# Performance work log

Measured on AMD Instinct MI355X. Metric: run time of the kernel, lower is better.

## Reference

```python
import jax, jax.numpy as jnp
import numpy as np

EPS = 1e-15
MAX_ATANH = 1.0 - 1e-5
V = 2097152   # total nodes (B*N*L flattened)
E = 8388608   # edges, ~avg degree 4 (temporal + parent/child)
ATT = 16
MAXD = 512    # mixer embedding table size
# curvature c = 1.0 (registered buffer, constant)


def _mobius_add(a, b):
    # Poincare ball Mobius addition, c = 1
    a2 = jnp.sum(a * a, -1, keepdims=True)
    b2 = jnp.sum(b * b, -1, keepdims=True)
    ab = jnp.sum(a * b, -1, keepdims=True)
    num = (1.0 + 2.0 * ab + b2) * a + (1.0 - a2) * b
    den = 1.0 + 2.0 * ab + a2 * b2
    return num / jnp.maximum(den, EPS)


def _log_map_x(x, y):
    # log_x(y): tangent vector at x pointing to y (c = 1)
    sub = _mobius_add(-x, y)
    n = jnp.maximum(jnp.linalg.norm(sub, axis=-1, keepdims=True), EPS)
    lam = 2.0 / jnp.maximum(1.0 - jnp.sum(x * x, -1, keepdims=True), EPS)
    return (2.0 / lam) * jnp.arctanh(jnp.minimum(n, MAX_ATANH)) * (sub / n)


def _exp_map_x(x, v):
    # exp_x(v) (c = 1)
    n = jnp.maximum(jnp.linalg.norm(v, axis=-1, keepdims=True), EPS)
    lam = 2.0 / jnp.maximum(1.0 - jnp.sum(x * x, -1, keepdims=True), EPS)
    return _mobius_add(x, jnp.tanh(0.5 * lam * n) * (v / n))


def setup_inputs() -> dict:
    key = jax.random.key(0)
    ks = jax.random.split(key, 8)
    # node embeddings strictly inside the unit ball: exp0 of a small tangent vec
    v0 = 0.5 * jax.random.normal(ks[0], (V, 2), jnp.float32)
    n0 = jnp.maximum(jnp.linalg.norm(v0, axis=-1, keepdims=True), EPS)
    x = jnp.tanh(n0) * v0 / n0
    edge_index = jax.random.randint(ks[1], (2, E), 0, V)
    depth = jax.random.randint(ks[2], (V,), 0, MAXD)
    W1 = jax.random.normal(ks[3], (2, ATT), jnp.float32) / jnp.sqrt(2.0)
    b1 = 0.1 * jax.random.normal(ks[4], (ATT,), jnp.float32)
    W2 = jax.random.normal(ks[5], (ATT, 1), jnp.float32) / jnp.sqrt(float(ATT))
    eta = jnp.float32(1.0)
    depth_scale = 1.0 + 0.01 * jax.random.normal(ks[6], (MAXD,), jnp.float32)
    depth_theta = 0.01 * jax.random.normal(ks[7], (MAXD,), jnp.float32)
    return {"x": x, "W1": W1, "b1": b1, "W2": W2, "eta": eta,
            "depth_scale": depth_scale, "depth_theta": depth_theta,
            "edge_index": edge_index, "depth": depth}


def reference(x, W1, b1, W2, eta, depth_scale, depth_theta, edge_index, depth):
    row, col = edge_index[0], edge_index[1]
    xi = x[row]                      # [E,2] gather target endpoints
    xj = x[col]                      # [E,2] gather source endpoints
    v_ij = _log_map_x(xi, xj)        # [E,2] hyperbolic log-map
    # small per-edge MLP scorer: Linear(2,16) -> GELU(exact) -> Linear(16,1)
    h = jax.nn.gelu(v_ij @ W1 + b1, approximate=False)
    scores = (h @ W2)[:, 0]          # [E]
    # segment softmax over target node (row)
    mx = jax.ops.segment_max(scores, row, num_segments=V)
    e = jnp.exp(scores - mx[row])
    den = jax.ops.segment_sum(e, row, num_segments=V)
    alpha = e / jnp.maximum(den[row], EPS)
    # scatter-add aggregate in tangent space
    m = jax.ops.segment_sum(alpha[:, None] * v_ij, row, num_segments=V)  # [V,2]
    # depth-gated mixer: per-node scale + 2D rotation
    d = jnp.minimum(depth, MAXD - 1)
    k = depth_scale[d][:, None]
    ang = depth_theta[d]
    ca, sa = jnp.cos(ang), jnp.sin(ang)
    m = k * jnp.stack([ca * m[:, 0] - sa * m[:, 1],
                       sa * m[:, 0] + ca * m[:, 1]], axis=-1)
    # exp-map update
    return _exp_map_x(x, eta * m)
```

## Files before the change

### kernel.cpp

```cpp
#include <hip/hip_runtime.h>
#include <math.h>

#define EPSF 1e-15f
#define MAX_ATANH (1.0f - 1e-5f)
#define ATT 16

#define LOG_NPB 11
#define NPB (1 << LOG_NPB)
#define MAXB 1024
#define NBLK 512
#define NPR 1024

#define TDIM 512
#define TSPAN 12.5f
#define TSTEP (TSPAN / (float)(TDIM - 1))
#define TSCALE ((float)(TDIM - 1) / TSPAN)
#define TOFF (6.25f * TSCALE)

__device__ __forceinline__ float fast_atanh(float z) {
    return 0.5f * __logf(__fdividef(1.0f + z, 1.0f - z));
}
__device__ __forceinline__ float fast_tanh(float z) {
    return 1.0f - __fdividef(2.0f, __expf(2.0f * z) + 1.0f);
}
__device__ __forceinline__ float gelu_exact(float u) {
    return 0.5f * u * (1.0f + erff(u * 0.70710678118654752f));
}

__global__ void __launch_bounds__(256) build_table_kernel(
        const float* __restrict__ W1, const float* __restrict__ b1,
        const float* __restrict__ W2, float2* __restrict__ tab) {
    const int idx = blockIdx.x * 256 + threadIdx.x;
    if (idx >= TDIM * TDIM) return;
    const int iy = idx >> 9;
    const int ix = idx & (TDIM - 1);
    const float vy  = fmaf((float)iy, TSTEP, -6.25f);
    const float vx0 = fmaf((float)ix, TSTEP, -6.25f);
    const float vx1 = fmaf((float)min(ix + 1, TDIM - 1), TSTEP, -6.25f);
    float s0 = 0.0f, s1 = 0.0f;
    #pragma unroll
    for (int k = 0; k < ATT; ++k) {
        const float w1x = W1[k], w1y = W1[ATT + k], bb = b1[k], w2 = W2[k];
        s0 = fmaf(gelu_exact(fmaf(vx0, w1x, fmaf(vy, w1y, bb))), w2, s0);
        s1 = fmaf(gelu_exact(fmaf(vx1, w1x, fmaf(vy, w1y, bb))), w2, s1);
    }
    tab[idx] = make_float2(s0, s1);
}

__global__ void __launch_bounds__(256) hist_kernel(const int* __restrict__ row,
                                                   int E, int B,
                                                   unsigned* __restrict__ counts ) {
    __shared__ unsigned h[MAXB];
    for (int i = threadIdx.x; i < B; i += 256) h[i] = 0u;
    __syncthreads();
    const int T = gridDim.x * 256;
    const int nv = E >> 2;
    const int4* row4 = (const int4*)row;
    for (int i = blockIdx.x * 256 + threadIdx.x; i < nv; i += T) {
        const int4 r = row4[i];
        atomicAdd(&h[((unsigned)r.x) >> LOG_NPB], 1u);
        atomicAdd(&h[((unsigned)r.y) >> LOG_NPB], 1u);
        atomicAdd(&h[((unsigned)r.z) >> LOG_NPB], 1u);
        atomicAdd(&h[((unsigned)r.w) >> LOG_NPB], 1u);
    }
    for (int e = (nv << 2) + blockIdx.x * 256 + threadIdx.x; e < E; e += T)
        atomicAdd(&h[((unsigned)row[e]) >> LOG_NPB], 1u);
    __syncthreads();
    for (int i = threadIdx.x; i < B; i += 256)
        counts[(size_t)i * gridDim.x + blockIdx.x] = h[i];
}

__global__ void __launch_bounds__(256) scan_blocks_kernel(const unsigned* __restrict__ counts,
                                                          unsigned* __restrict__ within,
                                                          unsigned* __restrict__ totals) {
    const int b = blockIdx.x;
    const unsigned* src = counts + (size_t)b * NBLK;
    unsigned* dst = within + (size_t)b * NBLK;
    __shared__ unsigned s[256];
    unsigned v0, v1;
    {
        const uint2 v = ((const uint2*)src)[threadIdx.x];
        v0 = v.x; v1 = v.y;
    }
    s[threadIdx.x] = v0 + v1;
    __syncthreads();
    for (int off = 1; off < 256; off <<= 1) {
        unsigned t = (threadIdx.x >= off) ? s[threadIdx.x - off] : 0u;
        __syncthreads();
        s[threadIdx.x] += t;
        __syncthreads();
    }
    unsigned base = (threadIdx.x > 0) ? s[threadIdx.x - 1] : 0u;
    uint2 o;
    o.x = base; o.y = base + v0;
    ((uint2*)dst)[threadIdx.x] = o;
    if (threadIdx.x == 255) totals[b] = s[255];
}

__global__ void __launch_bounds__(256) scan_totals_kernel(const unsigned* __restrict__ totals,
                                                          unsigned* __restrict__ base, int B) {
    __shared__ unsigned s[256];
    unsigned vals[8];
    const int i0 = threadIdx.x * 8;
    unsigned sum = 0u;
    #pragma unroll
    for (int k = 0; k < 8; ++k) {
        vals[k] = (i0 + k < B) ? totals[i0 + k] : 0u;
        sum += vals[k];
    }
    s[threadIdx.x] = sum;
    __syncthreads();
    for (int off = 1; off < 256; off <<= 1) {
        unsigned t = (threadIdx.x >= off) ? s[threadIdx.x - off] : 0u;
        __syncthreads();
        s[threadIdx.x] += t;
        __syncthreads();
    }
    unsigned b0 = (threadIdx.x > 0) ? s[threadIdx.x - 1] : 0u;
    #pragma unroll
    for (int k = 0; k < 8; ++k) {
        if (i0 + k < B) base[i0 + k] = b0;
        b0 += vals[k];
    }
    if (threadIdx.x == 255) base[B] = s[255];
}

__global__ void __launch_bounds__(256) scatter_kernel(const int* __restrict__ row,
                                                      const int* __restrict__ col,
                                                      int E, int B,
                                                      const unsigned* __restrict__ base,
                                                      const unsigned* __restrict__ within,
                                                      unsigned* __restrict__ payload) {
    __shared__ unsigned cur[MAXB];
    const int nblk = gridDim.x;
    for (int i = threadIdx.x; i < B; i += 256)
        cur[i] = base[i] + within[(size_t)i * nblk + blockIdx.x];
    __syncthreads();
    const int T = nblk * 256;
    const int nv = E >> 2;
    const int4* row4 = (const int4*)row;
    const int4* col4 = (const int4*)col;
    for (int i = blockIdx.x * 256 + threadIdx.x; i < nv; i += T) {
        const int4 r = row4[i];
        const int4 c = col4[i];
        {
            const unsigned rr = (unsigned)r.x;
            const unsigned pos = atomicAdd(&cur[rr >> LOG_NPB], 1u);
            payload[pos] = ((rr & (NPB - 1)) << 21) | (unsigned)c.x;
        }
        {
            const unsigned rr = (unsigned)r.y;
            const unsigned pos = atomicAdd(&cur[rr >> LOG_NPB], 1u);
            payload[pos] = ((rr & (NPB - 1)) << 21) | (unsigned)c.y;
        }
        {
            const unsigned rr = (unsigned)r.z;
            const unsigned pos = atomicAdd(&cur[rr >> LOG_NPB], 1u);
            payload[pos] = ((rr & (NPB - 1)) << 21) | (unsigned)c.z;
        }
        {
            const unsigned rr = (unsigned)r.w;
            const unsigned pos = atomicAdd(&cur[rr >> LOG_NPB], 1u);
            payload[pos] = ((rr & (NPB - 1)) << 21) | (unsigned)c.w;
        }
    }
    for (int e = (nv << 2) + blockIdx.x * 256 + threadIdx.x; e < E; e += T) {
        const unsigned rr = (unsigned)row[e];
        const unsigned pos = atomicAdd(&cur[rr >> LOG_NPB], 1u);
        payload[pos] = ((rr & (NPB - 1)) << 21) | (unsigned)col[e];
    }
}

__device__ __forceinline__ void edge_single(unsigned p,
        const float2* __restrict__ x, const float2* __restrict__ tab,
        const float2* sxi, float* sden, float* smx, float* smy) {
    const unsigned lrow = (p >> 21) & (NPR - 1);
    const unsigned c = p & 0x1FFFFFu;
    const float2 xj = x[c];
    const float2 xi = sxi[lrow];

    const float ax = -xi.x, ay = -xi.y;
    const float bx = xj.x,  by = xj.y;
    const float a2 = ax * ax + ay * ay;
    const float b2 = bx * bx + by * by;
    const float ab = ax * bx + ay * by;
    const float ca = 1.0f + 2.0f * ab + b2;
    const float cb = 1.0f - a2;
    const float dn = fmaxf(1.0f + 2.0f * ab + a2 * b2, EPSF);
    const float rdn = __fdividef(1.0f, dn);
    const float subx = (ca * ax + cb * bx) * rdn;
    const float suby = (ca * ay + cb * by) * rdn;

    const float n = fmaxf(sqrtf(subx * subx + suby * suby), EPSF);
    const float M = fmaxf(1.0f - (xi.x * xi.x + xi.y * xi.y), EPSF);
    const float scl = M * fast_atanh(fminf(n, MAX_ATANH)) * __fdividef(1.0f, n);
    const float vx = scl * subx;
    const float vy = scl * suby;

    float tx = fmaf(vx, TSCALE, TOFF);
    float ty = fmaf(vy, TSCALE, TOFF);
    tx = fminf(fmaxf(tx, 0.0f), 510.999f);
    ty = fminf(fmaxf(ty, 0.0f), 510.999f);
    const int ix = (int)tx;
    const int iy = (int)ty;
    const float fx = tx - (float)ix;
    const float fy = ty - (float)iy;
    const int baseIdx = (iy << 9) + ix;
    const float2 r0 = tab[baseIdx];
    const float2 r1 = tab[baseIdx + TDIM];
    const float s0 = fmaf(fx, r0.y - r0.x, r0.x);
    const float s1 = fmaf(fx, r1.y - r1.x, r1.x);
    const float s  = fmaf(fy, s1 - s0, s0);

    const float ee = __expf(s);
    atomicAdd(&sden[lrow], ee);
    atomicAdd(&smx[lrow], ee * vx);
    atomicAdd(&smy[lrow], ee * vy);
}

__global__ void __launch_bounds__(512, 8) bucket_reduce_kernel(
        const float2* __restrict__ x,
        const float2* __restrict__ tab,
        const unsigned* __restrict__ base,
        const unsigned* __restrict__ payload,
        const int* __restrict__ depth,
        const float* __restrict__ depth_scale,
        const float* __restrict__ depth_theta,
        const float* __restrict__ eta_p,
        float2* __restrict__ out, int V) {
    __shared__ float  sden[NPR];
    __shared__ float  smx[NPR];
    __shared__ float  smy[NPR];
    __shared__ float2 sxi[NPR];
    const int bkt = blockIdx.x >> 1;
    const unsigned hb = blockIdx.x & 1;
    const int nodeBase = (bkt << LOG_NPB) + ((int)hb << 10);
    for (int i = threadIdx.x; i < NPR; i += 512) {
        sden[i] = 0.f; smx[i] = 0.f; smy[i] = 0.f;
        sxi[i] = x[nodeBase + i];
    }
    __syncthreads();

    const unsigned e0 = base[bkt], e1 = base[bkt + 1];
    for (unsigned e = e0 + threadIdx.x; e < e1; e += 512) {
        const unsigned p = payload[e];
        if ((p >> 31) == hb)
            edge_single(p, x, tab, sxi, sden, smx, smy);
    }
    __syncthreads();

    const float eta = eta_p[0];
    for (int i = threadIdx.x; i < NPR; i += 512) {
        const int v = nodeBase + i;
        if (v >= V) break;
        const float rdv = __fdividef(1.0f, fmaxf(sden[i], EPSF));
        const float mx = smx[i] * rdv;
        const float my = smy[i] * rdv;

        const int d = min(depth[v], 511);
        const float k   = depth_scale[d];
        const float ang = depth_theta[d];
        const float cs = __cosf(ang), sn = __sinf(ang);
        const float m0 = eta * (k * (cs * mx - sn * my));
        const float m1 = eta * (k * (sn * mx + cs * my));

        const float2 xi = sxi[i];

        const float n = fmaxf(sqrtf(m0 * m0 + m1 * m1), EPSF);
        const float M = fmaxf(1.0f - (xi.x * xi.x + xi.y * xi.y), EPSF);
        const float t = fast_tanh(__fdividef(n, M));
        const float tn = t * __fdividef(1.0f, n);
        const float bx = tn * m0;
        const float by = tn * m1;

        const float a2 = xi.x * xi.x + xi.y * xi.y;
        const float b2 = bx * bx + by * by;
        const float ab = xi.x * bx + xi.y * by;
        const float ca = 1.0f + 2.0f * ab + b2;
        const float cb = 1.0f - a2;
        const float dn = fmaxf(1.0f + 2.0f * ab + a2 * b2, EPSF);
        const float rdn = __fdividef(1.0f, dn);

        out[v] = make_float2((ca * xi.x + cb * bx) * rdn,
                             (ca * xi.y + cb * by) * rdn);
    }
}

extern "C" void kernel_launch(void* const* d_in, const int* in_sizes, int n_in,
                              void* d_out, int out_size, void* d_ws, size_t ws_size,
                              hipStream_t stream) {
    const float2* x          = (const float2*)d_in[0];
    const float*  W1         = (const float*)d_in[1];
    const float*  b1         = (const float*)d_in[2];
    const float*  W2         = (const float*)d_in[3];
    const float*  eta        = (const float*)d_in[4];
    const float*  dscale     = (const float*)d_in[5];
    const float*  dtheta     = (const float*)d_in[6];
    const int*    edge_index = (const int*)d_in[7];
    const int*    depth      = (const int*)d_in[8];

    const int V = in_sizes[0] / 2;
    const int E = in_sizes[7] / 2;
    const int B = (V + NPB - 1) >> LOG_NPB;

    const int* row = edge_index;
    const int* col = edge_index + E;

    unsigned* payload = (unsigned*)d_ws;
    unsigned* counts  = payload + E;
    unsigned* within  = counts + (size_t)B * NBLK;
    unsigned* totals  = within + (size_t)B * NBLK;
    unsigned* base    = totals + B;
    float2*   tab     = (float2*)within;

    hist_kernel<<<NBLK, 256, 0, stream>>>(row, E, B, counts);
    scan_blocks_kernel<<<B, 256, 0, stream>>>(counts, within, totals);
    scan_totals_kernel<<<1, 256, 0, stream>>>(totals, base, B);
    scatter_kernel<<<NBLK, 256, 0, stream>>>(row, col, E, B, base, within, payload);
    build_table_kernel<<<(TDIM * TDIM) / 256, 256, 0, stream>>>(W1, b1, W2, tab);
    bucket_reduce_kernel<<<2 * B, 512, 0, stream>>>(x, tab, base, payload,
                                                    depth, dscale, dtheta, eta,
                                                    (float2*)d_out, V);
}
```

Measured before the change: 261.6 us.

## Split 2048-node buckets into 1024-node halves before reduction

Adds a split pass that partitions each 2048-node bucket's edge payload into two 1024-node sub-buckets using a finer histogram and scan. Each reduce block then reads only its own edges instead of scanning the whole bucket and discarding half. The aim is to remove the duplicated payload read and the divergent filter, at the cost of an extra kernel pass that reads and writes the full payload with contended shared atomics.

```diff
diff --git a/kernel.cpp b/kernel.cpp
--- a/kernel.cpp
+++ b/kernel.cpp
@@ -5,11 +5,13 @@
 #define MAX_ATANH (1.0f - 1e-5f)
 #define ATT 16
 
-#define LOG_NPB 11
-#define NPB (1 << LOG_NPB)
-#define MAXB 1024
+#define LOG_NPR 10
+#define NPR (1 << LOG_NPR)
+#define LOG_NPM 11
+#define NPM (1 << LOG_NPM)
+#define B2MAX 2048
+#define BMMAX 1024
 #define NBLK 512
-#define NPR 1024
 
 #define TDIM 512
 #define TSPAN 12.5f
@@ -48,41 +50,41 @@
 }
 
 __global__ void __launch_bounds__(256) hist_kernel(const int* __restrict__ row,
-                                                   int E, int B,
-                                                   unsigned* __restrict__ counts ) {
-    __shared__ unsigned h[MAXB];
-    for (int i = threadIdx.x; i < B; i += 256) h[i] = 0u;
+                                                   int E, int B2,
+                                                   unsigned* __restrict__ counts2 ) {
+    __shared__ unsigned h[B2MAX];
+    for (int i = threadIdx.x; i < B2; i += 256) h[i] = 0u;
     __syncthreads();
     const int T = gridDim.x * 256;
     const int nv = E >> 2;
     const int4* row4 = (const int4*)row;
     for (int i = blockIdx.x * 256 + threadIdx.x; i < nv; i += T) {
         const int4 r = row4[i];
-        atomicAdd(&h[((unsigned)r.x) >> LOG_NPB], 1u);
-        atomicAdd(&h[((unsigned)r.y) >> LOG_NPB], 1u);
-        atomicAdd(&h[((unsigned)r.z) >> LOG_NPB], 1u);
-        atomicAdd(&h[((unsigned)r.w) >> LOG_NPB], 1u);
+        atomicAdd(&h[((unsigned)r.x) >> LOG_NPR], 1u);
+        atomicAdd(&h[((unsigned)r.y) >> LOG_NPR], 1u);
+        atomicAdd(&h[((unsigned)r.z) >> LOG_NPR], 1u);
+        atomicAdd(&h[((unsigned)r.w) >> LOG_NPR], 1u);
     }
     for (int e = (nv << 2) + blockIdx.x * 256 + threadIdx.x; e < E; e += T)
-        atomicAdd(&h[((unsigned)row[e]) >> LOG_NPB], 1u);
-    __syncthreads();
-    for (int i = threadIdx.x; i < B; i += 256)
-        counts[(size_t)i * gridDim.x + blockIdx.x] = h[i];
-}
-
-__global__ void __launch_bounds__(256) scan_blocks_kernel(const unsigned* __restrict__ counts,
+        atomicAdd(&h[((unsigned)row[e]) >> LOG_NPR], 1u);
+    __syncthreads();
+    for (int i = threadIdx.x; i < B2; i += 256)
+        counts2[(size_t)i * gridDim.x + blockIdx.x] = h[i];
+}
+
+__global__ void __launch_bounds__(256) scan_blocks_kernel(const unsigned* __restrict__ counts2,
                                                           unsigned* __restrict__ within,
-                                                          unsigned* __restrict__ totals) {
+                                                          unsigned* __restrict__ totals2) {
     const int b = blockIdx.x;
-    const unsigned* src = counts + (size_t)b * NBLK;
-    unsigned* dst = within + (size_t)b * NBLK;
+    const uint2 r0 = ((const uint2*)(counts2 + (size_t)(2 * b)     * NBLK))[threadIdx.x];
+    const uint2 r1 = ((const uint2*)(counts2 + (size_t)(2 * b + 1) * NBLK))[threadIdx.x];
+    const unsigned c0 = r0.x + r1.x;
+    const unsigned c1 = r0.y + r1.y;
     __shared__ unsigned s[256];
-    unsigned v0, v1;
-    {
-        const uint2 v = ((const uint2*)src)[threadIdx.x];
-        v0 = v.x; v1 = v.y;
-    }
-    s[threadIdx.x] = v0 + v1;
+    __shared__ unsigned sa[256], sb[256];
+    s[threadIdx.x] = c0 + c1;
+    sa[threadIdx.x] = r0.x + r0.y;
+    sb[threadIdx.x] = r1.x + r1.y;
     __syncthreads();
     for (int off = 1; off < 256; off <<= 1) {
         unsigned t = (threadIdx.x >= off) ? s[threadIdx.x - off] : 0u;
@@ -92,20 +94,25 @@
     }
     unsigned base = (threadIdx.x > 0) ? s[threadIdx.x - 1] : 0u;
     uint2 o;
-    o.x = base; o.y = base + v0;
-    ((uint2*)dst)[threadIdx.x] = o;
-    if (threadIdx.x == 255) totals[b] = s[255];
-}
-
-__global__ void __launch_bounds__(256) scan_totals_kernel(const unsigned* __restrict__ totals,
-                                                          unsigned* __restrict__ base, int B) {
+    o.x = base; o.y = base + c0;
+    ((uint2*)(within + (size_t)b * NBLK))[threadIdx.x] = o;
+    for (int off = 128; off > 0; off >>= 1) {
+        if (threadIdx.x < off) { sa[threadIdx.x] += sa[threadIdx.x + off];
+                                 sb[threadIdx.x] += sb[threadIdx.x + off]; }
+        __syncthreads();
+    }
+    if (threadIdx.x == 0) { totals2[2 * b] = sa[0]; totals2[2 * b + 1] = sb[0]; }
+}
+
+__global__ void __launch_bounds__(256) scan_totals_kernel(const unsigned* __restrict__ totals2,
+                                                          unsigned* __restrict__ base2, int B2) {
     __shared__ unsigned s[256];
     unsigned vals[8];
     const int i0 = threadIdx.x * 8;
     unsigned sum = 0u;
     #pragma unroll
     for (int k = 0; k < 8; ++k) {
-        vals[k] = (i0 + k < B) ? totals[i0 + k] : 0u;
+        vals[k] = (i0 + k < B2) ? totals2[i0 + k] : 0u;
         sum += vals[k];
     }
     s[threadIdx.x] = sum;
@@ -119,22 +126,22 @@
     unsigned b0 = (threadIdx.x > 0) ? s[threadIdx.x - 1] : 0u;
     #pragma unroll
     for (int k = 0; k < 8; ++k) {
-        if (i0 + k < B) base[i0 + k] = b0;
+        if (i0 + k < B2) base2[i0 + k] = b0;
         b0 += vals[k];
     }
-    if (threadIdx.x == 255) base[B] = s[255];
+    if (threadIdx.x == 255) base2[B2] = s[255];
 }
 
 __global__ void __launch_bounds__(256) scatter_kernel(const int* __restrict__ row,
                                                       const int* __restrict__ col,
-                                                      int E, int B,
-                                                      const unsigned* __restrict__ base,
+                                                      int E, int BM,
+                                                      const unsigned* __restrict__ base2,
                                                       const unsigned* __restrict__ within,
                                                       unsigned* __restrict__ payload) {
-    __shared__ unsigned cur[MAXB];
+    __shared__ unsigned cur[BMMAX];
     const int nblk = gridDim.x;
-    for (int i = threadIdx.x; i < B; i += 256)
-        cur[i] = base[i] + within[(size_t)i * nblk + blockIdx.x];
+    for (int i = threadIdx.x; i < BM; i += 256)
+        cur[i] = base2[2 * i] + within[(size_t)i * nblk + blockIdx.x];
     __syncthreads();
     const int T = nblk * 256;
     const int nv = E >> 2;
@@ -145,36 +152,53 @@
         const int4 c = col4[i];
         {
             const unsigned rr = (unsigned)r.x;
-            const unsigned pos = atomicAdd(&cur[rr >> LOG_NPB], 1u);
-            payload[pos] = ((rr & (NPB - 1)) << 21) | (unsigned)c.x;
+            const unsigned pos = atomicAdd(&cur[rr >> LOG_NPM], 1u);
+            payload[pos] = ((rr & (NPM - 1)) << 21) | (unsigned)c.x;
         }
         {
             const unsigned rr = (unsigned)r.y;
-            const unsigned pos = atomicAdd(&cur[rr >> LOG_NPB], 1u);
-            payload[pos] = ((rr & (NPB - 1)) << 21) | (unsigned)c.y;
+            const unsigned pos = atomicAdd(&cur[rr >> LOG_NPM], 1u);
+            payload[pos] = ((rr & (NPM - 1)) << 21) | (unsigned)c.y;
         }
         {
             const unsigned rr = (unsigned)r.z;
-            const unsigned pos = atomicAdd(&cur[rr >> LOG_NPB], 1u);
-            payload[pos] = ((rr & (NPB - 1)) << 21) | (unsigned)c.z;
+            const unsigned pos = atomicAdd(&cur[rr >> LOG_NPM], 1u);
+            payload[pos] = ((rr & (NPM - 1)) << 21) | (unsigned)c.z;
         }
         {
             const unsigned rr = (unsigned)r.w;
-            const unsigned pos = atomicAdd(&cur[rr >> LOG_NPB], 1u);
-            payload[pos] = ((rr & (NPB - 1)) << 21) | (unsigned)c.w;
+            const unsigned pos = atomicAdd(&cur[rr >> LOG_NPM], 1u);
+            payload[pos] = ((rr & (NPM - 1)) << 21) | (unsigned)c.w;
         }
     }
     for (int e = (nv << 2) + blockIdx.x * 256 + threadIdx.x; e < E; e += T) {
         const unsigned rr = (unsigned)row[e];
-        const unsigned pos = atomicAdd(&cur[rr >> LOG_NPB], 1u);
-        payload[pos] = ((rr & (NPB - 1)) << 21) | (unsigned)col[e];
+        const unsigned pos = atomicAdd(&cur[rr >> LOG_NPM], 1u);
+        payload[pos] = ((rr & (NPM - 1)) << 21) | (unsigned)col[e];
+    }
+}
+
+__global__ void __launch_bounds__(256) split_kernel(const unsigned* __restrict__ base2,
+                                                    const unsigned* __restrict__ payload,
+                                                    unsigned* __restrict__ payload2) {
+    __shared__ unsigned cl, ch;
+    const int b = blockIdx.x;
+    if (threadIdx.x == 0) { cl = base2[2 * b]; ch = base2[2 * b + 1]; }
+    __syncthreads();
+    const unsigned e0 = base2[2 * b], e1 = base2[2 * b + 2];
+    for (unsigned e = e0 + threadIdx.x; e < e1; e += 256) {
+        const unsigned p = payload[e];
+        const unsigned lrow11 = p >> 21;
+        const unsigned dest = (lrow11 & NPR) ? atomicAdd(&ch, 1u)
+                                             : atomicAdd(&cl, 1u);
+        payload2[dest] = ((lrow11 & (NPR - 1)) << 21) | (p & 0x1FFFFFu);
     }
 }
 
 __device__ __forceinline__ void edge_single(unsigned p,
         const float2* __restrict__ x, const float2* __restrict__ tab,
         const float2* sxi, float* sden, float* smx, float* smy) {
-    const unsigned lrow = (p >> 21) & (NPR - 1);
+    const unsigned lrow = p >> 21;
     const unsigned c = p & 0x1FFFFFu;
     const float2 xj = x[c];
     const float2 xi = sxi[lrow];
@@ -221,8 +245,8 @@
 __global__ void __launch_bounds__(512, 8) bucket_reduce_kernel(
         const float2* __restrict__ x,
         const float2* __restrict__ tab,
-        const unsigned* __restrict__ base,
-        const unsigned* __restrict__ payload,
+        const unsigned* __restrict__ base2,
+        const unsigned* __restrict__ payload2,
         const int* __restrict__ depth,
         const float* __restrict__ depth_scale,
         const float* __restrict__ depth_theta,
@@ -232,21 +256,17 @@
     __shared__ float  smx[NPR];
     __shared__ float  smy[NPR];
     __shared__ float2 sxi[NPR];
-    const int bkt = blockIdx.x >> 1;
-    const unsigned hb = blockIdx.x & 1;
-    const int nodeBase = (bkt << LOG_NPB) + ((int)hb << 10);
+    const int b = blockIdx.x;
+    const int nodeBase = b << LOG_NPR;
     for (int i = threadIdx.x; i < NPR; i += 512) {
         sden[i] = 0.f; smx[i] = 0.f; smy[i] = 0.f;
         sxi[i] = x[nodeBase + i];
     }
     __syncthreads();
 
-    const unsigned e0 = base[bkt], e1 = base[bkt + 1];
-    for (unsigned e = e0 + threadIdx.x; e < e1; e += 512) {
-        const unsigned p = payload[e];
-        if ((p >> 31) == hb)
-            edge_single(p, x, tab, sxi, sden, smx, smy);
-    }
+    const unsigned e0 = base2[b], e1 = base2[b + 1];
+    for (unsigned e = e0 + threadIdx.x; e < e1; e += 512)
+        edge_single(payload2[e], x, tab, sxi, sden, smx, smy);
     __syncthreads();
 
     const float eta = eta_p[0];
@@ -301,24 +321,27 @@
 
     const int V = in_sizes[0] / 2;
     const int E = in_sizes[7] / 2;
-    const int B = (V + NPB - 1) >> LOG_NPB;
+    const int B2 = (V + NPR - 1) >> LOG_NPR;
+    const int BM = (V + NPM - 1) >> LOG_NPM;
 
     const int* row = edge_index;
     const int* col = edge_index + E;
 
-    unsigned* payload = (unsigned*)d_ws;
-    unsigned* counts  = payload + E;
-    unsigned* within  = counts + (size_t)B * NBLK;
-    unsigned* totals  = within + (size_t)B * NBLK;
-    unsigned* base    = totals + B;
-    float2*   tab     = (float2*)within;
-
-    hist_kernel<<<NBLK, 256, 0, stream>>>(row, E, B, counts);
-    scan_blocks_kernel<<<B, 256, 0, stream>>>(counts, within, totals);
-    scan_totals_kernel<<<1, 256, 0, stream>>>(totals, base, B);
-    scatter_kernel<<<NBLK, 256, 0, stream>>>(row, col, E, B, base, within, payload);
+    unsigned* payload  = (unsigned*)d_ws;
+    unsigned* payload2 = payload + (size_t)E;
+    unsigned* counts2  = payload2 + (size_t)E;
+    unsigned* within   = counts2 + (size_t)B2 * NBLK;
+    unsigned* totals2  = within + (size_t)BM * NBLK;
+    unsigned* base2    = totals2 + B2;
+    float2*   tab      = (float2*)counts2;
+
+    hist_kernel<<<NBLK, 256, 0, stream>>>(row, E, B2, counts2);
+    scan_blocks_kernel<<<BM, 256, 0, stream>>>(counts2, within, totals2);
+    scan_totals_kernel<<<1, 256, 0, stream>>>(totals2, base2, B2);
+    scatter_kernel<<<NBLK, 256, 0, stream>>>(row, col, E, BM, base2, within, payload);
+    split_kernel<<<BM, 256, 0, stream>>>(base2, payload, payload2);
     build_table_kernel<<<(TDIM * TDIM) / 256, 256, 0, stream>>>(W1, b1, W2, tab);
-    bucket_reduce_kernel<<<2 * B, 512, 0, stream>>>(x, tab, base, payload,
-                                                    depth, dscale, dtheta, eta,
-                                                    (float2*)d_out, V);
-}
+    bucket_reduce_kernel<<<B2, 512, 0, stream>>>(x, tab, base2, payload2,
+                                                 depth, dscale, dtheta, eta,
+                                                 (float2*)d_out, V);
+}
```

Result: slower. 284.4 us (+8.7%).
